# Kernel tuning notes

Measured on AMD Instinct MI355X. Metric: run time of the kernel, lower is better.

Reference implementation:

```python
import math
import jax, jax.numpy as jnp
import numpy as np

S, M, B, D, H = 256, 256, 8, 512, 8
HD = D // H
K = S + M  # key_len


def setup_inputs() -> dict:
    key = jax.random.key(0)
    ks = jax.random.split(key, 10)
    x = jax.random.normal(ks[0], (S, B, D), jnp.float32)
    memory = jax.random.normal(ks[1], (M, B, D), jnp.float32)
    rel_pos = jax.random.normal(ks[2], (K, D), jnp.float32)
    # causal mask: True means masked (key position after query position)
    q_pos = jnp.arange(S)[:, None] + M  # (S,1)
    k_pos = jnp.arange(K)[None, :]     # (1,K)
    attn_mask = jnp.broadcast_to(k_pos > q_pos, (B, S, K))
    scale = 1.0 / math.sqrt(D)
    Wq = jax.random.normal(ks[3], (D, D), jnp.float32) * scale
    Wk = jax.random.normal(ks[4], (D, D), jnp.float32) * scale
    Wv = jax.random.normal(ks[5], (D, D), jnp.float32) * scale
    Wr = jax.random.normal(ks[6], (D, D), jnp.float32) * scale
    Wo = jax.random.normal(ks[7], (D, D), jnp.float32) * scale
    u_bias = jax.random.normal(ks[8], (H, HD), jnp.float32) * 0.02
    v_bias = jax.random.normal(ks[9], (H, HD), jnp.float32) * 0.02
    return {"x": x, "memory": memory, "rel_pos": rel_pos, "attn_mask": attn_mask,
            "Wq": Wq, "Wk": Wk, "Wv": Wv, "Wr": Wr, "Wo": Wo,
            "u_bias": u_bias, "v_bias": v_bias}


def reference(x, memory, rel_pos, attn_mask, Wq, Wk, Wv, Wr, Wo, u_bias, v_bias):
    mem = jax.lax.stop_gradient(memory)
    kv = jnp.concatenate([mem, x], axis=0)  # (K, B, D)
    # projections (torch Linear: y = x @ W.T)
    q = (x @ Wq.T).reshape(S, B, H, HD).transpose(1, 2, 0, 3)   # (B,H,S,HD)
    k = (kv @ Wk.T).reshape(K, B, H, HD).transpose(1, 2, 0, 3)  # (B,H,K,HD)
    v = (kv @ Wv.T).reshape(K, B, H, HD).transpose(1, 2, 0, 3)  # (B,H,K,HD)
    r = (rel_pos[:K] @ Wr.T).reshape(K, H, HD)                  # (K,H,HD)
    # relative index gather
    q_pos = jnp.arange(S)[:, None] + M
    k_pos = jnp.arange(K)[None, :]
    rel_idx = jnp.clip(q_pos - k_pos, 0, K - 1)  # (S,K)
    r_qk = r[rel_idx]                            # (S,K,H,HD)
    qk = jnp.einsum('bhqd,bhkd->bhqk', q, k)
    qr = jnp.einsum('bhqd,qkhd->bhqk', q, r_qk)
    uk = jnp.einsum('hd,bhkd->bhk', u_bias, k)[:, :, None, :]
    vr = jnp.einsum('hd,qkhd->hqk', v_bias, r_qk)[None]
    scores = (qk + qr + uk + vr) / math.sqrt(HD)  # (B,H,S,K)
    scores = jnp.where(attn_mask[:, None, :, :], -jnp.inf, scores)
    weights = jax.nn.softmax(scores, axis=-1)
    y = jnp.einsum('bhqk,bhkd->bhqd', weights, v)
    y = y.transpose(2, 0, 1, 3).reshape(S, B, D)
    return y @ Wo.T
```

## Files before the change

### kernel.cpp

```cpp
#include <hip/hip_runtime.h>
#include <hip/hip_bf16.h>
#include <math.h>

constexpr int S_  = 256;
constexpr int Mm  = 256;
constexpr int Bb  = 8;
constexpr int Dd  = 512;
constexpr int Hh  = 8;
constexpr int HDd = 64;
constexpr int Kk  = 512;

typedef unsigned short u16;
typedef short bf16x8 __attribute__((ext_vector_type(8)));
typedef float f32x4  __attribute__((ext_vector_type(4)));

constexpr int LROW = 72;
constexpr int QSTR = 520;

__device__ __forceinline__ u16 f2b(float f) {
  __hip_bfloat16 h = __float2bfloat16(f);
  u16 b; __builtin_memcpy(&b, &h, 2); return b;
}
__device__ __forceinline__ unsigned int cvt2(float x, float y) {
  __hip_bfloat162 h = __float22bfloat162_rn(make_float2(x, y));
  unsigned int bits; __builtin_memcpy(&bits, &h, 4); return bits;
}
__device__ __forceinline__ float b2f(u16 b) {
  union { unsigned int u; float f; } v; v.u = ((unsigned int)b) << 16;
  return v.f;
}
__device__ __forceinline__ int4 pack8(float4 a, float4 b) {
  int4 r;
  r.x = (int)cvt2(a.x, a.y);
  r.y = (int)cvt2(a.z, a.w);
  r.z = (int)cvt2(b.x, b.y);
  r.w = (int)cvt2(b.z, b.w);
  return r;
}

__device__ __forceinline__ void stage_bf16(u16* dst, const u16* __restrict__ src,
                                           int ld, int tid) {
  const int r = tid >> 3, c = (tid & 7) * 8;
  *(int4*)(dst + r * LROW + c)        = *(const int4*)(src + (size_t)r * ld + c);
  *(int4*)(dst + (r + 32) * LROW + c) = *(const int4*)(src + (size_t)(r + 32) * ld + c);
}
__device__ __forceinline__ void stage_f32(u16* dst, const float* __restrict__ src,
                                          int ld, int tid, int nrow32) {
  const int r = tid >> 3, c = (tid & 7) * 8;
  for (int hh = 0; hh < nrow32; ++hh) {
    const float4 a = *(const float4*)(src + (size_t)(r + 32 * hh) * ld + c);
    const float4 b = *(const float4*)(src + (size_t)(r + 32 * hh) * ld + c + 4);
    *(int4*)(dst + (r + 32 * hh) * LROW + c) = pack8(a, b);
  }
}

__device__ __forceinline__ void mfma_step(const u16* As, const u16* Bs,
                                          f32x4 (&acc)[4], int wave, int lane) {
  const int r16 = lane & 15, q8 = (lane >> 4) * 8;
#pragma unroll
  for (int ks = 0; ks < 64; ks += 32) {
    const bf16x8 a = *(const bf16x8*)(As + (wave * 16 + r16) * LROW + ks + q8);
#pragma unroll
    for (int nb = 0; nb < 4; ++nb) {
      const bf16x8 b = *(const bf16x8*)(Bs + (nb * 16 + r16) * LROW + ks + q8);
      acc[nb] = __builtin_amdgcn_mfma_f32_16x16x32_bf16(a, b, acc[nb], 0, 0, 0);
    }
  }
}

__global__ __launch_bounds__(256) void k_proj(const float* __restrict__ x,
                                              const float* __restrict__ mem,
                                              const float* __restrict__ rel,
                                              const float* __restrict__ Wq,
                                              const float* __restrict__ Wk,
                                              const float* __restrict__ Wv,
                                              const float* __restrict__ Wr,
                                              const float* __restrict__ ub,
                                              const float* __restrict__ vb,
                                              u16* __restrict__ qu,
                                              u16* __restrict__ qv,
                                              u16* __restrict__ kb,
                                              u16* __restrict__ vT,
                                              u16* __restrict__ rT) {
  __shared__ u16 As[128 * LROW], Bs[64 * LROW], Bs2[64 * LROW];
  const int tid = threadIdx.x, wave = tid >> 6, lane = tid & 63;
  const int r16 = lane & 15, q8 = (lane >> 4) * 8, rq = (lane >> 4) * 4;
  const int sr = tid >> 3, scg = (tid & 7) * 8;
  const int bid = blockIdx.x;
  int kind, mt, nt;
  if (bid < 128)      { kind = 0; const int t = bid;       mt = t >> 3; nt = t & 7; }
  else if (bid < 384) { kind = 1; const int t = bid - 128; mt = t >> 3; nt = t & 7; }
  else                { kind = 2; const int t = bid - 384; mt = t >> 3; nt = t & 7; }
  const int m0 = mt * 128, n0 = nt * 64;
  const float *A, *B, *B2 = nullptr;
  if (kind == 0)      { A = x + (size_t)m0 * Dd; B = Wq + (size_t)n0 * Dd; }
  else if (kind == 1) { A = (m0 < Mm * Bb) ? mem + (size_t)m0 * Dd
                                           : x + (size_t)(m0 - Mm * Bb) * Dd;
                        B = Wk + (size_t)n0 * Dd; B2 = Wv + (size_t)n0 * Dd; }
  else                { A = rel + (size_t)m0 * Dd; B = Wr + (size_t)n0 * Dd; }

  f32x4 accK[2][4], accV[2][4];
#pragma unroll
  for (int mi = 0; mi < 2; ++mi)
#pragma unroll
    for (int nb = 0; nb < 4; ++nb) {
      accK[mi][nb] = (f32x4){0.f, 0.f, 0.f, 0.f};
      accV[mi][nb] = (f32x4){0.f, 0.f, 0.f, 0.f};
    }

  float4 fa[8], fb[4], fv[4];
#pragma unroll
  for (int hh = 0; hh < 4; ++hh) {
    fa[2 * hh]     = *(const float4*)(A + (size_t)(sr + 32 * hh) * Dd + scg);
    fa[2 * hh + 1] = *(const float4*)(A + (size_t)(sr + 32 * hh) * Dd + scg + 4);
  }
#pragma unroll
  for (int hh = 0; hh < 2; ++hh) {
    fb[2 * hh]     = *(const float4*)(B + (size_t)(sr + 32 * hh) * Dd + scg);
    fb[2 * hh + 1] = *(const float4*)(B + (size_t)(sr + 32 * hh) * Dd + scg + 4);
  }
  if (kind == 1) {
#pragma unroll
    for (int hh = 0; hh < 2; ++hh) {
      fv[2 * hh]     = *(const float4*)(B2 + (size_t)(sr + 32 * hh) * Dd + scg);
      fv[2 * hh + 1] = *(const float4*)(B2 + (size_t)(sr + 32 * hh) * Dd + scg + 4);
    }
  }
#pragma unroll
  for (int hh = 0; hh < 4; ++hh)
    *(int4*)(As + (sr + 32 * hh) * LROW + scg) = pack8(fa[2 * hh], fa[2 * hh + 1]);
#pragma unroll
  for (int hh = 0; hh < 2; ++hh)
    *(int4*)(Bs + (sr + 32 * hh) * LROW + scg) = pack8(fb[2 * hh], fb[2 * hh + 1]);
  if (kind == 1) {
#pragma unroll
    for (int hh = 0; hh < 2; ++hh)
      *(int4*)(Bs2 + (sr + 32 * hh) * LROW + scg) = pack8(fv[2 * hh], fv[2 * hh + 1]);
  }
  __syncthreads();

  for (int k0 = 0; k0 < Dd; k0 += 64) {
    const bool more = k0 < Dd - 64;
    if (more) {
      const int kn = k0 + 64;
#pragma unroll
      for (int hh = 0; hh < 4; ++hh) {
        fa[2 * hh]     = *(const float4*)(A + (size_t)(sr + 32 * hh) * Dd + kn + scg);
        fa[2 * hh + 1] = *(const float4*)(A + (size_t)(sr + 32 * hh) * Dd + kn + scg + 4);
      }
#pragma unroll
      for (int hh = 0; hh < 2; ++hh) {
        fb[2 * hh]     = *(const float4*)(B + (size_t)(sr + 32 * hh) * Dd + kn + scg);
        fb[2 * hh + 1] = *(const float4*)(B + (size_t)(sr + 32 * hh) * Dd + kn + scg + 4);
      }
      if (kind == 1) {
#pragma unroll
        for (int hh = 0; hh < 2; ++hh) {
          fv[2 * hh]     = *(const float4*)(B2 + (size_t)(sr + 32 * hh) * Dd + kn + scg);
          fv[2 * hh + 1] = *(const float4*)(B2 + (size_t)(sr + 32 * hh) * Dd + kn + scg + 4);
        }
      }
    }
#pragma unroll
    for (int ks = 0; ks < 64; ks += 32) {
      bf16x8 a[2];
#pragma unroll
      for (int mi = 0; mi < 2; ++mi)
        a[mi] = *(const bf16x8*)(As + (wave * 32 + mi * 16 + r16) * LROW + ks + q8);
#pragma unroll
      for (int nb = 0; nb < 4; ++nb) {
        const bf16x8 bk = *(const bf16x8*)(Bs + (nb * 16 + r16) * LROW + ks + q8);
#pragma unroll
        for (int mi = 0; mi < 2; ++mi)
          accK[mi][nb] = __builtin_amdgcn_mfma_f32_16x16x32_bf16(a[mi], bk, accK[mi][nb], 0, 0, 0);
        if (kind == 1) {
          const bf16x8 bv = *(const bf16x8*)(Bs2 + (nb * 16 + r16) * LROW + ks + q8);
#pragma unroll
          for (int mi = 0; mi < 2; ++mi)
            accV[mi][nb] = __builtin_amdgcn_mfma_f32_16x16x32_bf16(a[mi], bv, accV[mi][nb], 0, 0, 0);
        }
      }
    }
    __syncthreads();
    if (more) {
#pragma unroll
      for (int hh = 0; hh < 4; ++hh)
        *(int4*)(As + (sr + 32 * hh) * LROW + scg) = pack8(fa[2 * hh], fa[2 * hh + 1]);
#pragma unroll
      for (int hh = 0; hh < 2; ++hh)
        *(int4*)(Bs + (sr + 32 * hh) * LROW + scg) = pack8(fb[2 * hh], fb[2 * hh + 1]);
      if (kind == 1) {
#pragma unroll
        for (int hh = 0; hh < 2; ++hh)
          *(int4*)(Bs2 + (sr + 32 * hh) * LROW + scg) = pack8(fv[2 * hh], fv[2 * hh + 1]);
      }
      __syncthreads();
    }
  }

  const int h = n0 >> 6;
  if (kind == 0) {
#pragma unroll
    for (int nb = 0; nb < 4; ++nb) {
      const int hd = nb * 16 + r16, n = n0 + hd;
      const float u = ub[n], v = vb[n];
#pragma unroll
      for (int mi = 0; mi < 2; ++mi)
#pragma unroll
        for (int r = 0; r < 4; ++r) {
          const int m = m0 + wave * 32 + mi * 16 + rq + r;
          const int s = m >> 3, b = m & 7;
          const size_t d = ((size_t)(b * Hh + h) * S_ + s) * HDd + hd;
          qu[d] = f2b(accK[mi][nb][r] + u);
          qv[d] = f2b(accK[mi][nb][r] + v);
        }
    }
  } else if (kind == 1) {
#pragma unroll
    for (int nb = 0; nb < 4; ++nb) {
      const int hd = nb * 16 + r16;
#pragma unroll
      for (int mi = 0; mi < 2; ++mi)
#pragma unroll
        for (int r = 0; r < 4; ++r) {
          const int m = m0 + wave * 32 + mi * 16 + rq + r;
          const int pos = m >> 3, b = m & 7;
          kb[((size_t)(b * Hh + h) * Kk + pos) * HDd + hd] = f2b(accK[mi][nb][r]);
          vT[((size_t)(b * Hh + h) * HDd + hd) * Kk + pos] = f2b(accV[mi][nb][r]);
        }
    }
  } else {
#pragma unroll
    for (int nb = 0; nb < 4; ++nb) {
      const int hd = nb * 16 + r16;
#pragma unroll
      for (int mi = 0; mi < 2; ++mi)
#pragma unroll
        for (int r = 0; r < 4; ++r) {
          const int j = m0 + wave * 32 + mi * 16 + rq + r;
          rT[((size_t)h * Kk + j) * HDd + hd] = f2b(accK[mi][nb][r]);
        }
    }
  }
}

__global__ __launch_bounds__(256) void k_attn(const u16* __restrict__ qu,
                                              const u16* __restrict__ qv,
                                              const u16* __restrict__ kb,
                                              const u16* __restrict__ vT,
                                              const u16* __restrict__ rT,
                                              u16* __restrict__ y) {
  extern __shared__ u16 lds[];
  u16* QRP = lds;
  u16* Bs0 = lds + 64 * QSTR;
  u16* Bs1 = Bs0 + 64 * LROW;
  const int tid = threadIdx.x, wave = tid >> 6, lane = tid & 63;
  const int q0 = blockIdx.x * 64, bh = blockIdx.y, h = bh & 7, b = bh >> 3;
  const int r16 = lane & 15, q8 = (lane >> 4) * 8, rq = (lane >> 4) * 4;
  const int sr = tid >> 3, scg = (tid & 7) * 8;

  const u16* qvp = qv + ((size_t)bh * S_ + q0 + wave * 16 + r16) * HDd;
  const bf16x8 av0 = *(const bf16x8*)(qvp + q8);
  const bf16x8 av1 = *(const bf16x8*)(qvp + 32 + q8);
  const u16* qup = qu + ((size_t)bh * S_ + q0 + wave * 16 + r16) * HDd;
  const bf16x8 au0 = *(const bf16x8*)(qup + q8);
  const bf16x8 au1 = *(const bf16x8*)(qup + 32 + q8);

  const u16* rbase = rT + (size_t)h * Kk * HDd;
  const u16* kbase = kb + (size_t)bh * Kk * HDd;
  const u16* vbase = vT + (size_t)bh * HDd * Kk;

  f32x4 sc[8][4];
  f32x4 o[4];
#pragma unroll
  for (int nb = 0; nb < 4; ++nb) o[nb] = (f32x4){0.f, 0.f, 0.f, 0.f};
  float mx[4]  = {-INFINITY, -INFINITY, -INFINITY, -INFINITY};

  *(int4*)(Bs0 + sr * LROW + scg) =
      *(const int4*)(rbase + (size_t)sr * HDd + scg);
  *(int4*)(Bs0 + (sr + 32) * LROW + scg) =
      *(const int4*)(rbase + (size_t)(sr + 32) * HDd + scg);
  __syncthreads();

#pragma unroll
  for (int j = 0; j < 24; ++j) {
    int4 L0, L1;
    if (j < 23) {
      const int jn = j + 1;
      const u16* s;
      int ld;
      if (jn < 8)       { s = rbase + (size_t)(jn * 64) * HDd;       ld = HDd; }
      else if (jn < 16) { s = kbase + (size_t)((jn - 8) * 64) * HDd; ld = HDd; }
      else              { s = vbase + (jn - 16) * 64;                ld = Kk;  }
      L0 = *(const int4*)(s + (size_t)sr * ld + scg);
      L1 = *(const int4*)(s + (size_t)(sr + 32) * ld + scg);
    }
    const u16* buf = (j & 1) ? Bs1 : Bs0;

    if (j < 8) {
      f32x4 c4[4];
#pragma unroll
      for (int nb = 0; nb < 4; ++nb) c4[nb] = (f32x4){0.f, 0.f, 0.f, 0.f};
#pragma unroll
      for (int ks = 0; ks < 64; ks += 32) {
        const bf16x8 a = ks ? av1 : av0;
#pragma unroll
        for (int nb = 0; nb < 4; ++nb) {
          const bf16x8 bb = *(const bf16x8*)(buf + (nb * 16 + r16) * LROW + ks + q8);
          c4[nb] = __builtin_amdgcn_mfma_f32_16x16x32_bf16(a, bb, c4[nb], 0, 0, 0);
        }
      }
#pragma unroll
      for (int nb = 0; nb < 4; ++nb)
#pragma unroll
        for (int r = 0; r < 4; ++r)
          QRP[(wave * 16 + rq + r) * QSTR + j * 64 + nb * 16 + r16] = f2b(c4[nb][r]);
    } else if (j < 16) {
      const int t = j - 8;
#pragma unroll
      for (int nb = 0; nb < 4; ++nb) sc[t][nb] = (f32x4){0.f, 0.f, 0.f, 0.f};
#pragma unroll
      for (int ks = 0; ks < 64; ks += 32) {
        const bf16x8 a = ks ? au1 : au0;
#pragma unroll
        for (int nb = 0; nb < 4; ++nb) {
          const bf16x8 bb = *(const bf16x8*)(buf + (nb * 16 + r16) * LROW + ks + q8);
          sc[t][nb] = __builtin_amdgcn_mfma_f32_16x16x32_bf16(a, bb, sc[t][nb], 0, 0, 0);
        }
      }
      if (j == 15) {
#pragma unroll
        for (int kt = 0; kt < 8; ++kt)
#pragma unroll
          for (int nb = 0; nb < 4; ++nb) {
            const int kk = kt * 64 + nb * 16 + r16;
#pragma unroll
            for (int r = 0; r < 4; ++r) {
              const int ql = wave * 16 + rq + r;
              const int q  = q0 + ql;
              float v;
              if (kk <= q + Mm) {
                const float qr = b2f(QRP[ql * QSTR + (q + Mm - kk)]);
                v = (sc[kt][nb][r] + qr) * 0.125f;
              } else {
                v = -INFINITY;
              }
              sc[kt][nb][r] = v;
              mx[r] = fmaxf(mx[r], v);
            }
          }
#pragma unroll
        for (int r = 0; r < 4; ++r)
#pragma unroll
          for (int off = 1; off < 16; off <<= 1)
            mx[r] = fmaxf(mx[r], __shfl_xor(mx[r], off));
        float sum[4] = {0.f, 0.f, 0.f, 0.f};
#pragma unroll
        for (int kt = 0; kt < 8; ++kt)
#pragma unroll
          for (int nb = 0; nb < 4; ++nb)
#pragma unroll
            for (int r = 0; r < 4; ++r) {
              const float p = __expf(sc[kt][nb][r] - mx[r]);
              sc[kt][nb][r] = p;
              sum[r] += p;
            }
#pragma unroll
        for (int r = 0; r < 4; ++r)
#pragma unroll
          for (int off = 1; off < 16; off <<= 1) sum[r] += __shfl_xor(sum[r], off);
        float inv[4];
#pragma unroll
        for (int r = 0; r < 4; ++r) inv[r] = 1.0f / sum[r];
#pragma unroll
        for (int kt = 0; kt < 8; ++kt)
#pragma unroll
          for (int nb = 0; nb < 4; ++nb)
#pragma unroll
            for (int r = 0; r < 4; ++r)
              QRP[(wave * 16 + rq + r) * QSTR + kt * 64 + nb * 16 + r16] =
                  f2b(sc[kt][nb][r] * inv[r]);
      }
    } else {
      const int t = j - 16;
#pragma unroll
      for (int ks = 0; ks < 64; ks += 32) {
        const bf16x8 a = *(const bf16x8*)(QRP + (wave * 16 + r16) * QSTR + t * 64 + ks + q8);
#pragma unroll
        for (int nb = 0; nb < 4; ++nb) {
          const bf16x8 bb = *(const bf16x8*)(buf + (nb * 16 + r16) * LROW + ks + q8);
          o[nb] = __builtin_amdgcn_mfma_f32_16x16x32_bf16(a, bb, o[nb], 0, 0, 0);
        }
      }
    }

    if (j < 23) {
      u16* d = ((j + 1) & 1) ? Bs1 : Bs0;
      *(int4*)(d + sr * LROW + scg)        = L0;
      *(int4*)(d + (sr + 32) * LROW + scg) = L1;
    }
    __syncthreads();
  }

#pragma unroll
  for (int nb = 0; nb < 4; ++nb) {
    const int hd = nb * 16 + r16;
#pragma unroll
    for (int r = 0; r < 4; ++r) {
      const int q = q0 + wave * 16 + rq + r;
      y[((size_t)q * Bb + b) * Dd + h * HDd + hd] = f2b(o[nb][r]);
    }
  }
}

__global__ __launch_bounds__(256) void k_out(const u16* __restrict__ y,
                                             const float* __restrict__ Wo,
                                             float* __restrict__ out) {
  __shared__ u16 As[2][64 * LROW], Bs[2][64 * LROW];
  const int tid = threadIdx.x, wave = tid >> 6, lane = tid & 63;
  const int n0 = blockIdx.x * 64, m0 = blockIdx.y * 64;
  const int sr = tid >> 3, scg = (tid & 7) * 8;
  const u16* Ay = y + (size_t)m0 * Dd;
  const float* Bw = Wo + (size_t)n0 * Dd;
  f32x4 acc[4];
#pragma unroll
  for (int i = 0; i < 4; ++i) acc[i] = (f32x4){0.f, 0.f, 0.f, 0.f};

  stage_bf16(As[0], Ay, Dd, tid);
  stage_f32(Bs[0], Bw, Dd, tid, 2);
  __syncthreads();

#pragma unroll
  for (int t = 0; t < 8; ++t) {
    int4 La0, La1;
    float4 f0, f1, f2, f3;
    if (t < 7) {
      const u16* s = Ay + (t + 1) * 64;
      La0 = *(const int4*)(s + (size_t)sr * Dd + scg);
      La1 = *(const int4*)(s + (size_t)(sr + 32) * Dd + scg);
      const float* w = Bw + (t + 1) * 64;
      f0 = *(const float4*)(w + (size_t)sr * Dd + scg);
      f1 = *(const float4*)(w + (size_t)sr * Dd + scg + 4);
      f2 = *(const float4*)(w + (size_t)(sr + 32) * Dd + scg);
      f3 = *(const float4*)(w + (size_t)(sr + 32) * Dd + scg + 4);
    }
    mfma_step(As[t & 1], Bs[t & 1], acc, wave, lane);
    if (t < 7) {
      u16* da = As[(t + 1) & 1];
      *(int4*)(da + sr * LROW + scg)        = La0;
      *(int4*)(da + (sr + 32) * LROW + scg) = La1;
      u16* db = Bs[(t + 1) & 1];
      *(int4*)(db + sr * LROW + scg)        = pack8(f0, f1);
      *(int4*)(db + (sr + 32) * LROW + scg) = pack8(f2, f3);
    }
    __syncthreads();
  }

  const int r16 = lane & 15, rq = (lane >> 4) * 4;
#pragma unroll
  for (int nb = 0; nb < 4; ++nb) {
    const int n = n0 + nb * 16 + r16;
#pragma unroll
    for (int r = 0; r < 4; ++r) {
      const int m = m0 + wave * 16 + rq + r;
      out[(size_t)m * Dd + n] = acc[nb][r];
    }
  }
}

extern "C" void kernel_launch(void* const* d_in, const int* in_sizes, int n_in,
                              void* d_out, int out_size, void* d_ws, size_t ws_size,
                              hipStream_t stream) {
  const float* x    = (const float*)d_in[0];
  const float* mem  = (const float*)d_in[1];
  const float* rel  = (const float*)d_in[2];
  const float* Wq = (const float*)d_in[4];
  const float* Wk = (const float*)d_in[5];
  const float* Wv = (const float*)d_in[6];
  const float* Wr = (const float*)d_in[7];
  const float* Wo = (const float*)d_in[8];
  const float* ub = (const float*)d_in[9];
  const float* vb = (const float*)d_in[10];
  float* out = (float*)d_out;

  u16* qu = (u16*)d_ws;
  u16* qv = qu + 1048576;
  u16* kb = qv + 1048576;
  u16* vT = kb + 2097152;
  u16* rT = vT + 2097152;
  u16* yb = rT + 262144;

  constexpr int ATTN_LDS = (64 * QSTR + 2 * 64 * LROW) * (int)sizeof(u16);
  (void)hipFuncSetAttribute((const void*)k_attn,
                            hipFuncAttributeMaxDynamicSharedMemorySize, ATTN_LDS);

  k_proj<<<dim3(416),   dim3(256), 0,        stream>>>(x, mem, rel, Wq, Wk, Wv, Wr,
                                                       ub, vb, qu, qv, kb, vT, rT);
  k_attn<<<dim3(4, 64), dim3(256), ATTN_LDS, stream>>>(qu, qv, kb, vT, rT, yb);
  k_out <<<dim3(8, 32), dim3(256), 0,        stream>>>(yb, Wo, out);
}
```

Measured before the change: 135.9 us.

## Fuse R and K tile stages and prefetch V tiles into LDS during score phase

The attention kernel's 24-step single-tile pipeline becomes 8 steps that load R and K tiles together into a double buffer while prefetching V tiles into a dedicated LDS region, with the last two V tiles held in registers. The PV phase then runs from LDS with one barrier instead of one per tile. This cuts the number of barriers and global-load round trips. The cost is much larger LDS use and more register pressure, with launch bounds set to one block per SM, which lowers occupancy.

```diff
diff --git a/kernel.cpp b/kernel.cpp
--- a/kernel.cpp
+++ b/kernel.cpp
@@ -244,16 +244,17 @@
   }
 }
 
-__global__ __launch_bounds__(256) void k_attn(const u16* __restrict__ qu,
-                                              const u16* __restrict__ qv,
-                                              const u16* __restrict__ kb,
-                                              const u16* __restrict__ vT,
-                                              const u16* __restrict__ rT,
-                                              u16* __restrict__ y) {
+__global__ __launch_bounds__(256, 1) void k_attn(const u16* __restrict__ qu,
+                                                 const u16* __restrict__ qv,
+                                                 const u16* __restrict__ kb,
+                                                 const u16* __restrict__ vT,
+                                                 const u16* __restrict__ rT,
+                                                 u16* __restrict__ y) {
   extern __shared__ u16 lds[];
   u16* QRP = lds;
-  u16* Bs0 = lds + 64 * QSTR;
-  u16* Bs1 = Bs0 + 64 * LROW;
+  u16* VS  = lds + 64 * QSTR;
+  u16* KR0 = VS + 6 * 64 * LROW;
+  u16* KR1 = KR0 + 128 * LROW;
   const int tid = threadIdx.x, wave = tid >> 6, lane = tid & 63;
   const int q0 = blockIdx.x * 64, bh = blockIdx.y, h = bh & 7, b = bh >> 3;
   const int r16 = lane & 15, q8 = (lane >> 4) * 8, rq = (lane >> 4) * 4;
@@ -274,132 +275,177 @@
   f32x4 o[4];
 #pragma unroll
   for (int nb = 0; nb < 4; ++nb) o[nb] = (f32x4){0.f, 0.f, 0.f, 0.f};
-  float mx[4]  = {-INFINITY, -INFINITY, -INFINITY, -INFINITY};
-
-  *(int4*)(Bs0 + sr * LROW + scg) =
+  float mx[4] = {-INFINITY, -INFINITY, -INFINITY, -INFINITY};
+
+  *(int4*)(KR0 + sr * LROW + scg) =
       *(const int4*)(rbase + (size_t)sr * HDd + scg);
-  *(int4*)(Bs0 + (sr + 32) * LROW + scg) =
+  *(int4*)(KR0 + (sr + 32) * LROW + scg) =
       *(const int4*)(rbase + (size_t)(sr + 32) * HDd + scg);
+  *(int4*)(KR0 + (64 + sr) * LROW + scg) =
+      *(const int4*)(kbase + (size_t)sr * HDd + scg);
+  *(int4*)(KR0 + (64 + sr + 32) * LROW + scg) =
+      *(const int4*)(kbase + (size_t)(sr + 32) * HDd + scg);
   __syncthreads();
 
-#pragma unroll
-  for (int j = 0; j < 24; ++j) {
-    int4 L0, L1;
-    if (j < 23) {
-      const int jn = j + 1;
-      const u16* s;
-      int ld;
-      if (jn < 8)       { s = rbase + (size_t)(jn * 64) * HDd;       ld = HDd; }
-      else if (jn < 16) { s = kbase + (size_t)((jn - 8) * 64) * HDd; ld = HDd; }
-      else              { s = vbase + (jn - 16) * 64;                ld = Kk;  }
-      L0 = *(const int4*)(s + (size_t)sr * ld + scg);
-      L1 = *(const int4*)(s + (size_t)(sr + 32) * ld + scg);
-    }
-    const u16* buf = (j & 1) ? Bs1 : Bs0;
-
-    if (j < 8) {
-      f32x4 c4[4];
-#pragma unroll
-      for (int nb = 0; nb < 4; ++nb) c4[nb] = (f32x4){0.f, 0.f, 0.f, 0.f};
-#pragma unroll
-      for (int ks = 0; ks < 64; ks += 32) {
-        const bf16x8 a = ks ? av1 : av0;
-#pragma unroll
-        for (int nb = 0; nb < 4; ++nb) {
-          const bf16x8 bb = *(const bf16x8*)(buf + (nb * 16 + r16) * LROW + ks + q8);
-          c4[nb] = __builtin_amdgcn_mfma_f32_16x16x32_bf16(a, bb, c4[nb], 0, 0, 0);
+  int4 V6a, V6b, V7a, V7b;
+
+#pragma unroll
+  for (int t = 0; t < 8; ++t) {
+    const u16* buf = (t & 1) ? KR1 : KR0;
+    u16* nxt      = (t & 1) ? KR0 : KR1;
+    int4 Lr0, Lr1, Lk0, Lk1, Lv0, Lv1;
+    if (t < 7) {
+      const u16* rs = rbase + (size_t)((t + 1) * 64) * HDd;
+      Lr0 = *(const int4*)(rs + (size_t)sr * HDd + scg);
+      Lr1 = *(const int4*)(rs + (size_t)(sr + 32) * HDd + scg);
+      const u16* ks = kbase + (size_t)((t + 1) * 64) * HDd;
+      Lk0 = *(const int4*)(ks + (size_t)sr * HDd + scg);
+      Lk1 = *(const int4*)(ks + (size_t)(sr + 32) * HDd + scg);
+    }
+    if (t < 6) {
+      const u16* vs = vbase + t * 64;
+      Lv0 = *(const int4*)(vs + (size_t)sr * Kk + scg);
+      Lv1 = *(const int4*)(vs + (size_t)(sr + 32) * Kk + scg);
+    } else if (t == 6) {
+      const u16* vs = vbase + 6 * 64;
+      V6a = *(const int4*)(vs + (size_t)sr * Kk + scg);
+      V6b = *(const int4*)(vs + (size_t)(sr + 32) * Kk + scg);
+    } else {
+      const u16* vs = vbase + 7 * 64;
+      V7a = *(const int4*)(vs + (size_t)sr * Kk + scg);
+      V7b = *(const int4*)(vs + (size_t)(sr + 32) * Kk + scg);
+    }
+
+    f32x4 c4[4];
+#pragma unroll
+    for (int nb = 0; nb < 4; ++nb) c4[nb] = (f32x4){0.f, 0.f, 0.f, 0.f};
+#pragma unroll
+    for (int ks = 0; ks < 64; ks += 32) {
+      const bf16x8 a = ks ? av1 : av0;
+#pragma unroll
+      for (int nb = 0; nb < 4; ++nb) {
+        const bf16x8 bb = *(const bf16x8*)(buf + (nb * 16 + r16) * LROW + ks + q8);
+        c4[nb] = __builtin_amdgcn_mfma_f32_16x16x32_bf16(a, bb, c4[nb], 0, 0, 0);
+      }
+    }
+#pragma unroll
+    for (int nb = 0; nb < 4; ++nb)
+#pragma unroll
+      for (int r = 0; r < 4; ++r)
+        QRP[(wave * 16 + rq + r) * QSTR + t * 64 + nb * 16 + r16] = f2b(c4[nb][r]);
+
+#pragma unroll
+    for (int nb = 0; nb < 4; ++nb) sc[t][nb] = (f32x4){0.f, 0.f, 0.f, 0.f};
+#pragma unroll
+    for (int ks = 0; ks < 64; ks += 32) {
+      const bf16x8 a = ks ? au1 : au0;
+#pragma unroll
+      for (int nb = 0; nb < 4; ++nb) {
+        const bf16x8 bb = *(const bf16x8*)(buf + (64 + nb * 16 + r16) * LROW + ks + q8);
+        sc[t][nb] = __builtin_amdgcn_mfma_f32_16x16x32_bf16(a, bb, sc[t][nb], 0, 0, 0);
+      }
+    }
+
+    if (t < 7) {
+      *(int4*)(nxt + sr * LROW + scg)             = Lr0;
+      *(int4*)(nxt + (sr + 32) * LROW + scg)      = Lr1;
+      *(int4*)(nxt + (64 + sr) * LROW + scg)      = Lk0;
+      *(int4*)(nxt + (64 + sr + 32) * LROW + scg) = Lk1;
+    }
+    if (t < 6) {
+      u16* vd = VS + t * (64 * LROW);
+      *(int4*)(vd + sr * LROW + scg)        = Lv0;
+      *(int4*)(vd + (sr + 32) * LROW + scg) = Lv1;
+    }
+    __syncthreads();
+  }
+
+#pragma unroll
+  for (int kt = 0; kt < 8; ++kt)
+#pragma unroll
+    for (int nb = 0; nb < 4; ++nb) {
+      const int kk = kt * 64 + nb * 16 + r16;
+#pragma unroll
+      for (int r = 0; r < 4; ++r) {
+        const int ql = wave * 16 + rq + r;
+        const int q  = q0 + ql;
+        float v;
+        if (kk <= q + Mm) {
+          const float qr = b2f(QRP[ql * QSTR + (q + Mm - kk)]);
+          v = (sc[kt][nb][r] + qr) * 0.125f;
+        } else {
+          v = -INFINITY;
         }
-      }
-#pragma unroll
-      for (int nb = 0; nb < 4; ++nb)
-#pragma unroll
-        for (int r = 0; r < 4; ++r)
-          QRP[(wave * 16 + rq + r) * QSTR + j * 64 + nb * 16 + r16] = f2b(c4[nb][r]);
-    } else if (j < 16) {
-      const int t = j - 8;
-#pragma unroll
-      for (int nb = 0; nb < 4; ++nb) sc[t][nb] = (f32x4){0.f, 0.f, 0.f, 0.f};
-#pragma unroll
-      for (int ks = 0; ks < 64; ks += 32) {
-        const bf16x8 a = ks ? au1 : au0;
-#pragma unroll
-        for (int nb = 0; nb < 4; ++nb) {
-          const bf16x8 bb = *(const bf16x8*)(buf + (nb * 16 + r16) * LROW + ks + q8);
-          sc[t][nb] = __builtin_amdgcn_mfma_f32_16x16x32_bf16(a, bb, sc[t][nb], 0, 0, 0);
-        }
-      }
-      if (j == 15) {
-#pragma unroll
-        for (int kt = 0; kt < 8; ++kt)
-#pragma unroll
-          for (int nb = 0; nb < 4; ++nb) {
-            const int kk = kt * 64 + nb * 16 + r16;
-#pragma unroll
-            for (int r = 0; r < 4; ++r) {
-              const int ql = wave * 16 + rq + r;
-              const int q  = q0 + ql;
-              float v;
-              if (kk <= q + Mm) {
-                const float qr = b2f(QRP[ql * QSTR + (q + Mm - kk)]);
-                v = (sc[kt][nb][r] + qr) * 0.125f;
-              } else {
-                v = -INFINITY;
-              }
-              sc[kt][nb][r] = v;
-              mx[r] = fmaxf(mx[r], v);
-            }
-          }
-#pragma unroll
-        for (int r = 0; r < 4; ++r)
-#pragma unroll
-          for (int off = 1; off < 16; off <<= 1)
-            mx[r] = fmaxf(mx[r], __shfl_xor(mx[r], off));
-        float sum[4] = {0.f, 0.f, 0.f, 0.f};
-#pragma unroll
-        for (int kt = 0; kt < 8; ++kt)
-#pragma unroll
-          for (int nb = 0; nb < 4; ++nb)
-#pragma unroll
-            for (int r = 0; r < 4; ++r) {
-              const float p = __expf(sc[kt][nb][r] - mx[r]);
-              sc[kt][nb][r] = p;
-              sum[r] += p;
-            }
-#pragma unroll
-        for (int r = 0; r < 4; ++r)
-#pragma unroll
-          for (int off = 1; off < 16; off <<= 1) sum[r] += __shfl_xor(sum[r], off);
-        float inv[4];
-#pragma unroll
-        for (int r = 0; r < 4; ++r) inv[r] = 1.0f / sum[r];
-#pragma unroll
-        for (int kt = 0; kt < 8; ++kt)
-#pragma unroll
-          for (int nb = 0; nb < 4; ++nb)
-#pragma unroll
-            for (int r = 0; r < 4; ++r)
-              QRP[(wave * 16 + rq + r) * QSTR + kt * 64 + nb * 16 + r16] =
-                  f2b(sc[kt][nb][r] * inv[r]);
-      }
-    } else {
-      const int t = j - 16;
-#pragma unroll
-      for (int ks = 0; ks < 64; ks += 32) {
-        const bf16x8 a = *(const bf16x8*)(QRP + (wave * 16 + r16) * QSTR + t * 64 + ks + q8);
-#pragma unroll
-        for (int nb = 0; nb < 4; ++nb) {
-          const bf16x8 bb = *(const bf16x8*)(buf + (nb * 16 + r16) * LROW + ks + q8);
-          o[nb] = __builtin_amdgcn_mfma_f32_16x16x32_bf16(a, bb, o[nb], 0, 0, 0);
-        }
-      }
-    }
-
-    if (j < 23) {
-      u16* d = ((j + 1) & 1) ? Bs1 : Bs0;
-      *(int4*)(d + sr * LROW + scg)        = L0;
-      *(int4*)(d + (sr + 32) * LROW + scg) = L1;
-    }
-    __syncthreads();
+        sc[kt][nb][r] = v;
+        mx[r] = fmaxf(mx[r], v);
+      }
+    }
+#pragma unroll
+  for (int r = 0; r < 4; ++r)
+#pragma unroll
+    for (int off = 1; off < 16; off <<= 1)
+      mx[r] = fmaxf(mx[r], __shfl_xor(mx[r], off));
+  float sum[4] = {0.f, 0.f, 0.f, 0.f};
+#pragma unroll
+  for (int kt = 0; kt < 8; ++kt)
+#pragma unroll
+    for (int nb = 0; nb < 4; ++nb)
+#pragma unroll
+      for (int r = 0; r < 4; ++r) {
+        const float p = __expf(sc[kt][nb][r] - mx[r]);
+        sc[kt][nb][r] = p;
+        sum[r] += p;
+      }
+#pragma unroll
+  for (int r = 0; r < 4; ++r)
+#pragma unroll
+    for (int off = 1; off < 16; off <<= 1) sum[r] += __shfl_xor(sum[r], off);
+  float inv[4];
+#pragma unroll
+  for (int r = 0; r < 4; ++r) inv[r] = 1.0f / sum[r];
+#pragma unroll
+  for (int kt = 0; kt < 8; ++kt)
+#pragma unroll
+    for (int nb = 0; nb < 4; ++nb)
+#pragma unroll
+      for (int r = 0; r < 4; ++r)
+        QRP[(wave * 16 + rq + r) * QSTR + kt * 64 + nb * 16 + r16] =
+            f2b(sc[kt][nb][r] * inv[r]);
+
+#pragma unroll
+  for (int t = 0; t < 6; ++t) {
+    if (t == 0) {
+      *(int4*)(KR0 + sr * LROW + scg)        = V6a;
+      *(int4*)(KR0 + (sr + 32) * LROW + scg) = V6b;
+    }
+    if (t == 1) {
+      *(int4*)(KR1 + sr * LROW + scg)        = V7a;
+      *(int4*)(KR1 + (sr + 32) * LROW + scg) = V7b;
+    }
+    const u16* vs = VS + t * (64 * LROW);
+#pragma unroll
+    for (int ks = 0; ks < 64; ks += 32) {
+      const bf16x8 a = *(const bf16x8*)(QRP + (wave * 16 + r16) * QSTR + t * 64 + ks + q8);
+#pragma unroll
+      for (int nb = 0; nb < 4; ++nb) {
+        const bf16x8 bb = *(const bf16x8*)(vs + (nb * 16 + r16) * LROW + ks + q8);
+        o[nb] = __builtin_amdgcn_mfma_f32_16x16x32_bf16(a, bb, o[nb], 0, 0, 0);
+      }
+    }
+  }
+  __syncthreads();
+#pragma unroll
+  for (int t = 6; t < 8; ++t) {
+    const u16* vs = (t == 6) ? KR0 : KR1;
+#pragma unroll
+    for (int ks = 0; ks < 64; ks += 32) {
+      const bf16x8 a = *(const bf16x8*)(QRP + (wave * 16 + r16) * QSTR + t * 64 + ks + q8);
+#pragma unroll
+      for (int nb = 0; nb < 4; ++nb) {
+        const bf16x8 bb = *(const bf16x8*)(vs + (nb * 16 + r16) * LROW + ks + q8);
+        o[nb] = __builtin_amdgcn_mfma_f32_16x16x32_bf16(a, bb, o[nb], 0, 0, 0);
+      }
+    }
   }
 
 #pragma unroll
@@ -490,7 +536,8 @@
   u16* rT = vT + 2097152;
   u16* yb = rT + 262144;
 
-  constexpr int ATTN_LDS = (64 * QSTR + 2 * 64 * LROW) * (int)sizeof(u16);
+  constexpr int ATTN_LDS =
+      (64 * QSTR + 6 * 64 * LROW + 2 * 128 * LROW) * (int)sizeof(u16);
   (void)hipFuncSetAttribute((const void*)k_attn,
                             hipFuncAttributeMaxDynamicSharedMemorySize, ATTN_LDS);
 
```

Measured after the change: 133.7 us. About the same (-1.6%).

## Skip causally masked key tiles and load MFMA operands directly from global

Applied to the files above, without the earlier changes.

The attention kernel now computes only the key tiles a query block can see under the causal mask, (q0/64)+5 of the 8 tiles, in the QR, QK and PV stages. It drops the double-buffered LDS staging and per-tile __syncthreads, and reads the B fragments for R, K and V straight from global memory into registers. This shrinks LDS use and adds a launch-bounds hint of two blocks per CU to raise occupancy. The cost is uncoalesced per-lane global loads that rely on cache hits, and uninitialised score tiles that depend on the mask forcing them to -inf.

```diff
diff --git a/kernel.cpp b/kernel.cpp
--- a/kernel.cpp
+++ b/kernel.cpp
@@ -244,20 +244,18 @@
   }
 }
 
-__global__ __launch_bounds__(256) void k_attn(const u16* __restrict__ qu,
-                                              const u16* __restrict__ qv,
-                                              const u16* __restrict__ kb,
-                                              const u16* __restrict__ vT,
-                                              const u16* __restrict__ rT,
-                                              u16* __restrict__ y) {
+__global__ __launch_bounds__(256, 2) void k_attn(const u16* __restrict__ qu,
+                                                 const u16* __restrict__ qv,
+                                                 const u16* __restrict__ kb,
+                                                 const u16* __restrict__ vT,
+                                                 const u16* __restrict__ rT,
+                                                 u16* __restrict__ y) {
   extern __shared__ u16 lds[];
   u16* QRP = lds;
-  u16* Bs0 = lds + 64 * QSTR;
-  u16* Bs1 = Bs0 + 64 * LROW;
   const int tid = threadIdx.x, wave = tid >> 6, lane = tid & 63;
   const int q0 = blockIdx.x * 64, bh = blockIdx.y, h = bh & 7, b = bh >> 3;
   const int r16 = lane & 15, q8 = (lane >> 4) * 8, rq = (lane >> 4) * 4;
-  const int sr = tid >> 3, scg = (tid & 7) * 8;
+  const int ntiles = (q0 >> 6) + 5;
 
   const u16* qvp = qv + ((size_t)bh * S_ + q0 + wave * 16 + r16) * HDd;
   const bf16x8 av0 = *(const bf16x8*)(qvp + q8);
@@ -266,140 +264,112 @@
   const bf16x8 au0 = *(const bf16x8*)(qup + q8);
   const bf16x8 au1 = *(const bf16x8*)(qup + 32 + q8);
 
-  const u16* rbase = rT + (size_t)h * Kk * HDd;
-  const u16* kbase = kb + (size_t)bh * Kk * HDd;
-  const u16* vbase = vT + (size_t)bh * HDd * Kk;
+  const u16* rfrag = rT + (size_t)h * Kk * HDd + (size_t)r16 * HDd;
+  const u16* kfrag = kb + (size_t)bh * Kk * HDd + (size_t)r16 * HDd;
+  const u16* vfrag = vT + (size_t)bh * HDd * Kk + (size_t)r16 * Kk;
 
   f32x4 sc[8][4];
   f32x4 o[4];
 #pragma unroll
   for (int nb = 0; nb < 4; ++nb) o[nb] = (f32x4){0.f, 0.f, 0.f, 0.f};
-  float mx[4]  = {-INFINITY, -INFINITY, -INFINITY, -INFINITY};
-
-  *(int4*)(Bs0 + sr * LROW + scg) =
-      *(const int4*)(rbase + (size_t)sr * HDd + scg);
-  *(int4*)(Bs0 + (sr + 32) * LROW + scg) =
-      *(const int4*)(rbase + (size_t)(sr + 32) * HDd + scg);
-  __syncthreads();
-
-#pragma unroll
-  for (int j = 0; j < 24; ++j) {
-    int4 L0, L1;
-    if (j < 23) {
-      const int jn = j + 1;
-      const u16* s;
-      int ld;
-      if (jn < 8)       { s = rbase + (size_t)(jn * 64) * HDd;       ld = HDd; }
-      else if (jn < 16) { s = kbase + (size_t)((jn - 8) * 64) * HDd; ld = HDd; }
-      else              { s = vbase + (jn - 16) * 64;                ld = Kk;  }
-      L0 = *(const int4*)(s + (size_t)sr * ld + scg);
-      L1 = *(const int4*)(s + (size_t)(sr + 32) * ld + scg);
-    }
-    const u16* buf = (j & 1) ? Bs1 : Bs0;
-
-    if (j < 8) {
-      f32x4 c4[4];
-#pragma unroll
-      for (int nb = 0; nb < 4; ++nb) c4[nb] = (f32x4){0.f, 0.f, 0.f, 0.f};
-#pragma unroll
-      for (int ks = 0; ks < 64; ks += 32) {
-        const bf16x8 a = ks ? av1 : av0;
-#pragma unroll
-        for (int nb = 0; nb < 4; ++nb) {
-          const bf16x8 bb = *(const bf16x8*)(buf + (nb * 16 + r16) * LROW + ks + q8);
-          c4[nb] = __builtin_amdgcn_mfma_f32_16x16x32_bf16(a, bb, c4[nb], 0, 0, 0);
-        }
-      }
-#pragma unroll
-      for (int nb = 0; nb < 4; ++nb)
-#pragma unroll
-        for (int r = 0; r < 4; ++r)
-          QRP[(wave * 16 + rq + r) * QSTR + j * 64 + nb * 16 + r16] = f2b(c4[nb][r]);
-    } else if (j < 16) {
-      const int t = j - 8;
-#pragma unroll
-      for (int nb = 0; nb < 4; ++nb) sc[t][nb] = (f32x4){0.f, 0.f, 0.f, 0.f};
-#pragma unroll
-      for (int ks = 0; ks < 64; ks += 32) {
-        const bf16x8 a = ks ? au1 : au0;
-#pragma unroll
-        for (int nb = 0; nb < 4; ++nb) {
-          const bf16x8 bb = *(const bf16x8*)(buf + (nb * 16 + r16) * LROW + ks + q8);
-          sc[t][nb] = __builtin_amdgcn_mfma_f32_16x16x32_bf16(a, bb, sc[t][nb], 0, 0, 0);
-        }
-      }
-      if (j == 15) {
-#pragma unroll
-        for (int kt = 0; kt < 8; ++kt)
-#pragma unroll
-          for (int nb = 0; nb < 4; ++nb) {
-            const int kk = kt * 64 + nb * 16 + r16;
-#pragma unroll
-            for (int r = 0; r < 4; ++r) {
-              const int ql = wave * 16 + rq + r;
-              const int q  = q0 + ql;
-              float v;
-              if (kk <= q + Mm) {
-                const float qr = b2f(QRP[ql * QSTR + (q + Mm - kk)]);
-                v = (sc[kt][nb][r] + qr) * 0.125f;
-              } else {
-                v = -INFINITY;
-              }
-              sc[kt][nb][r] = v;
-              mx[r] = fmaxf(mx[r], v);
-            }
-          }
-#pragma unroll
-        for (int r = 0; r < 4; ++r)
-#pragma unroll
-          for (int off = 1; off < 16; off <<= 1)
-            mx[r] = fmaxf(mx[r], __shfl_xor(mx[r], off));
-        float sum[4] = {0.f, 0.f, 0.f, 0.f};
-#pragma unroll
-        for (int kt = 0; kt < 8; ++kt)
-#pragma unroll
-          for (int nb = 0; nb < 4; ++nb)
-#pragma unroll
-            for (int r = 0; r < 4; ++r) {
-              const float p = __expf(sc[kt][nb][r] - mx[r]);
-              sc[kt][nb][r] = p;
-              sum[r] += p;
-            }
-#pragma unroll
-        for (int r = 0; r < 4; ++r)
-#pragma unroll
-          for (int off = 1; off < 16; off <<= 1) sum[r] += __shfl_xor(sum[r], off);
-        float inv[4];
-#pragma unroll
-        for (int r = 0; r < 4; ++r) inv[r] = 1.0f / sum[r];
-#pragma unroll
-        for (int kt = 0; kt < 8; ++kt)
-#pragma unroll
-          for (int nb = 0; nb < 4; ++nb)
-#pragma unroll
-            for (int r = 0; r < 4; ++r)
-              QRP[(wave * 16 + rq + r) * QSTR + kt * 64 + nb * 16 + r16] =
-                  f2b(sc[kt][nb][r] * inv[r]);
-      }
-    } else {
-      const int t = j - 16;
-#pragma unroll
-      for (int ks = 0; ks < 64; ks += 32) {
-        const bf16x8 a = *(const bf16x8*)(QRP + (wave * 16 + r16) * QSTR + t * 64 + ks + q8);
-#pragma unroll
-        for (int nb = 0; nb < 4; ++nb) {
-          const bf16x8 bb = *(const bf16x8*)(buf + (nb * 16 + r16) * LROW + ks + q8);
-          o[nb] = __builtin_amdgcn_mfma_f32_16x16x32_bf16(a, bb, o[nb], 0, 0, 0);
-        }
-      }
-    }
-
-    if (j < 23) {
-      u16* d = ((j + 1) & 1) ? Bs1 : Bs0;
-      *(int4*)(d + sr * LROW + scg)        = L0;
-      *(int4*)(d + (sr + 32) * LROW + scg) = L1;
-    }
-    __syncthreads();
+  float mx[4] = {-INFINITY, -INFINITY, -INFINITY, -INFINITY};
+
+#pragma unroll
+  for (int t = 0; t < 8; ++t) if (t < ntiles) {
+    f32x4 c4[4];
+#pragma unroll
+    for (int nb = 0; nb < 4; ++nb) c4[nb] = (f32x4){0.f, 0.f, 0.f, 0.f};
+#pragma unroll
+    for (int ks = 0; ks < 64; ks += 32) {
+      const bf16x8 a = ks ? av1 : av0;
+#pragma unroll
+      for (int nb = 0; nb < 4; ++nb) {
+        const bf16x8 bb = *(const bf16x8*)(rfrag + (size_t)(t * 64 + nb * 16) * HDd + ks + q8);
+        c4[nb] = __builtin_amdgcn_mfma_f32_16x16x32_bf16(a, bb, c4[nb], 0, 0, 0);
+      }
+    }
+#pragma unroll
+    for (int nb = 0; nb < 4; ++nb)
+#pragma unroll
+      for (int r = 0; r < 4; ++r)
+        QRP[(wave * 16 + rq + r) * QSTR + t * 64 + nb * 16 + r16] = f2b(c4[nb][r]);
+
+#pragma unroll
+    for (int nb = 0; nb < 4; ++nb) sc[t][nb] = (f32x4){0.f, 0.f, 0.f, 0.f};
+#pragma unroll
+    for (int ks = 0; ks < 64; ks += 32) {
+      const bf16x8 a = ks ? au1 : au0;
+#pragma unroll
+      for (int nb = 0; nb < 4; ++nb) {
+        const bf16x8 bb = *(const bf16x8*)(kfrag + (size_t)(t * 64 + nb * 16) * HDd + ks + q8);
+        sc[t][nb] = __builtin_amdgcn_mfma_f32_16x16x32_bf16(a, bb, sc[t][nb], 0, 0, 0);
+      }
+    }
+  }
+
+#pragma unroll
+  for (int kt = 0; kt < 8; ++kt)
+#pragma unroll
+    for (int nb = 0; nb < 4; ++nb) {
+      const int kk = kt * 64 + nb * 16 + r16;
+#pragma unroll
+      for (int r = 0; r < 4; ++r) {
+        const int ql = wave * 16 + rq + r;
+        const int q  = q0 + ql;
+        float v;
+        if (kk <= q + Mm) {
+          const float qr = b2f(QRP[ql * QSTR + (q + Mm - kk)]);
+          v = (sc[kt][nb][r] + qr) * 0.125f;
+        } else {
+          v = -INFINITY;
+        }
+        sc[kt][nb][r] = v;
+        mx[r] = fmaxf(mx[r], v);
+      }
+    }
+#pragma unroll
+  for (int r = 0; r < 4; ++r)
+#pragma unroll
+    for (int off = 1; off < 16; off <<= 1)
+      mx[r] = fmaxf(mx[r], __shfl_xor(mx[r], off));
+  float sum[4] = {0.f, 0.f, 0.f, 0.f};
+#pragma unroll
+  for (int kt = 0; kt < 8; ++kt)
+#pragma unroll
+    for (int nb = 0; nb < 4; ++nb)
+#pragma unroll
+      for (int r = 0; r < 4; ++r) {
+        const float p = __expf(sc[kt][nb][r] - mx[r]);
+        sc[kt][nb][r] = p;
+        sum[r] += p;
+      }
+#pragma unroll
+  for (int r = 0; r < 4; ++r)
+#pragma unroll
+    for (int off = 1; off < 16; off <<= 1) sum[r] += __shfl_xor(sum[r], off);
+  float inv[4];
+#pragma unroll
+  for (int r = 0; r < 4; ++r) inv[r] = 1.0f / sum[r];
+#pragma unroll
+  for (int kt = 0; kt < 8; ++kt)
+#pragma unroll
+    for (int nb = 0; nb < 4; ++nb)
+#pragma unroll
+      for (int r = 0; r < 4; ++r)
+        QRP[(wave * 16 + rq + r) * QSTR + kt * 64 + nb * 16 + r16] =
+            f2b(sc[kt][nb][r] * inv[r]);
+
+#pragma unroll
+  for (int t = 0; t < 8; ++t) if (t < ntiles) {
+#pragma unroll
+    for (int ks = 0; ks < 64; ks += 32) {
+      const bf16x8 a = *(const bf16x8*)(QRP + (wave * 16 + r16) * QSTR + t * 64 + ks + q8);
+#pragma unroll
+      for (int nb = 0; nb < 4; ++nb) {
+        const bf16x8 bb = *(const bf16x8*)(vfrag + (size_t)(nb * 16) * Kk + t * 64 + ks + q8);
+        o[nb] = __builtin_amdgcn_mfma_f32_16x16x32_bf16(a, bb, o[nb], 0, 0, 0);
+      }
+    }
   }
 
 #pragma unroll
@@ -490,7 +460,7 @@
   u16* rT = vT + 2097152;
   u16* yb = rT + 262144;
 
-  constexpr int ATTN_LDS = (64 * QSTR + 2 * 64 * LROW) * (int)sizeof(u16);
+  constexpr int ATTN_LDS = 64 * QSTR * (int)sizeof(u16);
   (void)hipFuncSetAttribute((const void*)k_attn,
                             hipFuncAttributeMaxDynamicSharedMemorySize, ATTN_LDS);
 
```

New measurement: 146.9 us. 8.1% more time.

## Swizzle attention LDS layouts, drop padding, and reorder block indexing

Applied to the files above, without the earlier changes.

Replaces the padded LDS rows (stride 520 and 72) with unpadded rows whose 8-element groups are XOR-swizzled by row, to avoid bank conflicts while shrinking shared memory. The attention grid is flattened so consecutive blocks cover different heads and batches of the same query tile. A launch bound of 2 blocks per CU is added so more blocks can be resident. The risks are extra index arithmetic and register pressure from the occupancy hint, since the kernel holds a large score array in registers.

```diff
diff --git a/kernel.cpp b/kernel.cpp
--- a/kernel.cpp
+++ b/kernel.cpp
@@ -15,7 +15,6 @@
 typedef float f32x4  __attribute__((ext_vector_type(4)));
 
 constexpr int LROW = 72;
-constexpr int QSTR = 520;
 
 __device__ __forceinline__ u16 f2b(float f) {
   __hip_bfloat16 h = __float2bfloat16(f);
@@ -36,6 +35,16 @@
   r.z = (int)cvt2(b.x, b.y);
   r.w = (int)cvt2(b.z, b.w);
   return r;
+}
+
+__device__ __forceinline__ int qofs(int row, int col) {
+  return row * 512 + ((((col >> 3) ^ (row & 7)) << 3) | (col & 7));
+}
+__device__ __forceinline__ int qofs8(int row, int col8) {
+  return row * 512 + (((col8 >> 3) ^ (row & 7)) << 3);
+}
+__device__ __forceinline__ int sofs(int row, int col8) {
+  return row * 64 + (((col8 >> 3) ^ (row & 7)) << 3);
 }
 
 __device__ __forceinline__ void stage_bf16(u16* dst, const u16* __restrict__ src,
@@ -244,18 +253,20 @@
   }
 }
 
-__global__ __launch_bounds__(256) void k_attn(const u16* __restrict__ qu,
-                                              const u16* __restrict__ qv,
-                                              const u16* __restrict__ kb,
-                                              const u16* __restrict__ vT,
-                                              const u16* __restrict__ rT,
-                                              u16* __restrict__ y) {
+__global__ __launch_bounds__(256, 2) void k_attn(const u16* __restrict__ qu,
+                                                 const u16* __restrict__ qv,
+                                                 const u16* __restrict__ kb,
+                                                 const u16* __restrict__ vT,
+                                                 const u16* __restrict__ rT,
+                                                 u16* __restrict__ y) {
   extern __shared__ u16 lds[];
   u16* QRP = lds;
-  u16* Bs0 = lds + 64 * QSTR;
-  u16* Bs1 = Bs0 + 64 * LROW;
+  u16* Bs0 = lds + 64 * 512;
+  u16* Bs1 = Bs0 + 64 * 64;
   const int tid = threadIdx.x, wave = tid >> 6, lane = tid & 63;
-  const int q0 = blockIdx.x * 64, bh = blockIdx.y, h = bh & 7, b = bh >> 3;
+  const int bid = blockIdx.x;
+  const int h = bid & 7, b = (bid >> 3) & 7, q0 = (bid >> 6) * 64;
+  const int bh = b * Hh + h;
   const int r16 = lane & 15, q8 = (lane >> 4) * 8, rq = (lane >> 4) * 4;
   const int sr = tid >> 3, scg = (tid & 7) * 8;
 
@@ -270,15 +281,21 @@
   const u16* kbase = kb + (size_t)bh * Kk * HDd;
   const u16* vbase = vT + (size_t)bh * HDd * Kk;
 
+  auto tsrc = [&](int jj, const u16*& s, int& ld) {
+    if (jj < 8)       { s = rbase + (size_t)(jj * 64) * HDd;       ld = HDd; }
+    else if (jj < 16) { s = kbase + (size_t)((jj - 8) * 64) * HDd; ld = HDd; }
+    else              { s = vbase + (jj - 16) * 64;                ld = Kk;  }
+  };
+
   f32x4 sc[8][4];
   f32x4 o[4];
 #pragma unroll
   for (int nb = 0; nb < 4; ++nb) o[nb] = (f32x4){0.f, 0.f, 0.f, 0.f};
-  float mx[4]  = {-INFINITY, -INFINITY, -INFINITY, -INFINITY};
-
-  *(int4*)(Bs0 + sr * LROW + scg) =
+  float mx[4] = {-INFINITY, -INFINITY, -INFINITY, -INFINITY};
+
+  *(int4*)(Bs0 + sofs(sr, scg)) =
       *(const int4*)(rbase + (size_t)sr * HDd + scg);
-  *(int4*)(Bs0 + (sr + 32) * LROW + scg) =
+  *(int4*)(Bs0 + sofs(sr + 32, scg)) =
       *(const int4*)(rbase + (size_t)(sr + 32) * HDd + scg);
   __syncthreads();
 
@@ -286,12 +303,7 @@
   for (int j = 0; j < 24; ++j) {
     int4 L0, L1;
     if (j < 23) {
-      const int jn = j + 1;
-      const u16* s;
-      int ld;
-      if (jn < 8)       { s = rbase + (size_t)(jn * 64) * HDd;       ld = HDd; }
-      else if (jn < 16) { s = kbase + (size_t)((jn - 8) * 64) * HDd; ld = HDd; }
-      else              { s = vbase + (jn - 16) * 64;                ld = Kk;  }
+      const u16* s; int ld; tsrc(j + 1, s, ld);
       L0 = *(const int4*)(s + (size_t)sr * ld + scg);
       L1 = *(const int4*)(s + (size_t)(sr + 32) * ld + scg);
     }
@@ -306,7 +318,7 @@
         const bf16x8 a = ks ? av1 : av0;
 #pragma unroll
         for (int nb = 0; nb < 4; ++nb) {
-          const bf16x8 bb = *(const bf16x8*)(buf + (nb * 16 + r16) * LROW + ks + q8);
+          const bf16x8 bb = *(const bf16x8*)(buf + sofs(nb * 16 + r16, ks + q8));
           c4[nb] = __builtin_amdgcn_mfma_f32_16x16x32_bf16(a, bb, c4[nb], 0, 0, 0);
         }
       }
@@ -314,7 +326,7 @@
       for (int nb = 0; nb < 4; ++nb)
 #pragma unroll
         for (int r = 0; r < 4; ++r)
-          QRP[(wave * 16 + rq + r) * QSTR + j * 64 + nb * 16 + r16] = f2b(c4[nb][r]);
+          QRP[qofs(wave * 16 + rq + r, j * 64 + nb * 16 + r16)] = f2b(c4[nb][r]);
     } else if (j < 16) {
       const int t = j - 8;
 #pragma unroll
@@ -324,7 +336,7 @@
         const bf16x8 a = ks ? au1 : au0;
 #pragma unroll
         for (int nb = 0; nb < 4; ++nb) {
-          const bf16x8 bb = *(const bf16x8*)(buf + (nb * 16 + r16) * LROW + ks + q8);
+          const bf16x8 bb = *(const bf16x8*)(buf + sofs(nb * 16 + r16, ks + q8));
           sc[t][nb] = __builtin_amdgcn_mfma_f32_16x16x32_bf16(a, bb, sc[t][nb], 0, 0, 0);
         }
       }
@@ -340,7 +352,7 @@
               const int q  = q0 + ql;
               float v;
               if (kk <= q + Mm) {
-                const float qr = b2f(QRP[ql * QSTR + (q + Mm - kk)]);
+                const float qr = b2f(QRP[qofs(ql, q + Mm - kk)]);
                 v = (sc[kt][nb][r] + qr) * 0.125f;
               } else {
                 v = -INFINITY;
@@ -378,17 +390,17 @@
           for (int nb = 0; nb < 4; ++nb)
 #pragma unroll
             for (int r = 0; r < 4; ++r)
-              QRP[(wave * 16 + rq + r) * QSTR + kt * 64 + nb * 16 + r16] =
+              QRP[qofs(wave * 16 + rq + r, kt * 64 + nb * 16 + r16)] =
                   f2b(sc[kt][nb][r] * inv[r]);
       }
     } else {
       const int t = j - 16;
 #pragma unroll
       for (int ks = 0; ks < 64; ks += 32) {
-        const bf16x8 a = *(const bf16x8*)(QRP + (wave * 16 + r16) * QSTR + t * 64 + ks + q8);
+        const bf16x8 a = *(const bf16x8*)(QRP + qofs8(wave * 16 + r16, t * 64 + ks + q8));
 #pragma unroll
         for (int nb = 0; nb < 4; ++nb) {
-          const bf16x8 bb = *(const bf16x8*)(buf + (nb * 16 + r16) * LROW + ks + q8);
+          const bf16x8 bb = *(const bf16x8*)(buf + sofs(nb * 16 + r16, ks + q8));
           o[nb] = __builtin_amdgcn_mfma_f32_16x16x32_bf16(a, bb, o[nb], 0, 0, 0);
         }
       }
@@ -396,8 +408,8 @@
 
     if (j < 23) {
       u16* d = ((j + 1) & 1) ? Bs1 : Bs0;
-      *(int4*)(d + sr * LROW + scg)        = L0;
-      *(int4*)(d + (sr + 32) * LROW + scg) = L1;
+      *(int4*)(d + sofs(sr, scg))      = L0;
+      *(int4*)(d + sofs(sr + 32, scg)) = L1;
     }
     __syncthreads();
   }
@@ -490,12 +502,12 @@
   u16* rT = vT + 2097152;
   u16* yb = rT + 262144;
 
-  constexpr int ATTN_LDS = (64 * QSTR + 2 * 64 * LROW) * (int)sizeof(u16);
+  constexpr int ATTN_LDS = (64 * 512 + 2 * 64 * 64) * (int)sizeof(u16);
   (void)hipFuncSetAttribute((const void*)k_attn,
                             hipFuncAttributeMaxDynamicSharedMemorySize, ATTN_LDS);
 
   k_proj<<<dim3(416),   dim3(256), 0,        stream>>>(x, mem, rel, Wq, Wk, Wv, Wr,
                                                        ub, vb, qu, qv, kb, vT, rT);
-  k_attn<<<dim3(4, 64), dim3(256), ATTN_LDS, stream>>>(qu, qv, kb, vT, rT, yb);
+  k_attn<<<dim3(256),   dim3(256), ATTN_LDS, stream>>>(qu, qv, kb, vT, rT, yb);
   k_out <<<dim3(8, 32), dim3(256), 0,        stream>>>(yb, Wo, out);
 }
```

Result: slower. 163.4 us (+20.3%).
